# Kernel tuning notes

Hardware: AMD Instinct MI355X
Metric: run time of the kernel (lower is better)

## Reference

```python
import jax, jax.numpy as jnp
import numpy as np

N_NODES = 50000


def _degree_norms(edge_index, n_nodes):
    # PyG GCNConv: add self-loops, deg = 1 + in-degree at target (col)
    src, dst = edge_index[0], edge_index[1]
    deg = 1.0 + jax.ops.segment_sum(jnp.ones(src.shape[0], jnp.float32), dst,
                                    num_segments=n_nodes)
    d_inv_sqrt = 1.0 / jnp.sqrt(deg)  # deg >= 1 always (self-loop)
    norm_e = d_inv_sqrt[src] * d_inv_sqrt[dst]   # per-edge sym norm
    norm_self = d_inv_sqrt * d_inv_sqrt          # self-loop weight
    return norm_e, norm_self


def _gcn_conv(x, W, b, src, dst, norm_e, norm_self, n_nodes):
    h = x @ W                                    # [N, F_out]
    msg = h[src] * norm_e[:, None]               # gather + scale, [E, F_out]
    agg = jax.ops.segment_sum(msg, dst, num_segments=n_nodes)
    return agg + norm_self[:, None] * h + b


def setup_inputs() -> dict:
    key = jax.random.key(0)
    ks = jax.random.split(key, 10)
    F_in, H = 128, 128
    E = 1_600_000
    x = jax.random.normal(ks[0], (N_NODES, F_in), jnp.float32)
    edge_index = jax.random.randint(ks[1], (2, E), 0, N_NODES, dtype=jnp.int64)

    def glorot(k, fi, fo):
        s = jnp.sqrt(6.0 / (fi + fo)).astype(jnp.float32)
        return jax.random.uniform(k, (fi, fo), jnp.float32, -s, s)

    return {
        "x": x,
        "edge_index": edge_index,
        "W1": glorot(ks[2], F_in, H), "b1": jnp.zeros((H,), jnp.float32),
        "W2": glorot(ks[3], H, H),    "b2": jnp.zeros((H,), jnp.float32),
        "W3": glorot(ks[4], H, H),    "b3": jnp.zeros((H,), jnp.float32),
        "W4": glorot(ks[5], H, 1),    "b4": jnp.zeros((1,), jnp.float32),
    }


def reference(x, edge_index, W1, b1, W2, b2, W3, b3, W4, b4):
    src, dst = edge_index[0], edge_index[1]
    norm_e, norm_self = _degree_norms(edge_index, N_NODES)
    h = jax.nn.relu(_gcn_conv(x, W1, b1, src, dst, norm_e, norm_self, N_NODES))
    h = jax.nn.relu(_gcn_conv(h, W2, b2, src, dst, norm_e, norm_self, N_NODES))
    h = jax.nn.relu(_gcn_conv(h, W3, b3, src, dst, norm_e, norm_self, N_NODES))
    return _gcn_conv(h, W4, b4, src, dst, norm_e, norm_self, N_NODES)
```

## Files before the change

kernel.cpp:

```cpp
#include <hip/hip_runtime.h>
#include <hip/hip_bf16.h>
#include <stdint.h>

typedef unsigned int u32;
typedef unsigned short u16;

#define F 128

typedef __attribute__((ext_vector_type(8))) short bf16x8;
typedef __attribute__((ext_vector_type(4))) float f32x4;

__device__ __forceinline__ float bf2f(u16 v){
  union { u32 u; float f; } x; x.u = ((u32)v) << 16; return x.f;
}
__device__ __forceinline__ u16 f2bf(float f){
  union { float f; u32 u; } x; x.f = f;
  u32 u = x.u;
  return (u16)((u + 0x7fffu + ((u >> 16) & 1u)) >> 16);
}

__global__ void k_dtype(const u32* __restrict__ w, int nwords, int* __restrict__ isf32){
  u32 hit = 0;
  for (int i = threadIdx.x; i < nwords; i += blockDim.x){
    u32 e = (w[i] >> 7) & 0xFFu;
    if (e > 160u) hit = 1;
  }
  if (hit) atomicOr(isf32, 1);
}

__global__ void k_detect(const u32* __restrict__ w, int ncheck, int* __restrict__ flag){
  u32 v = 0;
  for (int i = threadIdx.x; i < ncheck; i += blockDim.x) v |= w[2*i + 1];
  if (v) atomicOr(flag, 1);
}

__launch_bounds__(256)
__global__ void k_bhist(const u32* __restrict__ w, int E, const int* __restrict__ flagp,
                        int NB, int* __restrict__ bcnt){
  __shared__ int h[256];
  int st = (*flagp) ? 1 : 2;
  int t = threadIdx.x;
  h[t] = 0;
  __syncthreads();
  int base = blockIdx.x*4096;
  #pragma unroll 4
  for (int k = 0; k < 16; k++){
    int i = base + k*256 + t;
    if (i < E){
      int d = (int)w[(size_t)(E + i)*st];
      atomicAdd(&h[d >> 8], 1);
    }
  }
  __syncthreads();
  if (t < NB && h[t]) atomicAdd(&bcnt[t], h[t]);
}

__global__ void k_bscan(const int* __restrict__ bcnt, int NB, int E,
                        int* __restrict__ bbase, int* __restrict__ bump){
  __shared__ int s[256];
  int t = threadIdx.x;
  int v = (t < NB) ? bcnt[t] : 0;
  s[t] = v;
  __syncthreads();
  for (int off = 1; off < 256; off <<= 1){
    int x = (t >= off) ? s[t - off] : 0;
    __syncthreads();
    s[t] += x;
    __syncthreads();
  }
  bbase[t] = s[t] - v;
  if (t == 255) bbase[256] = E;
  bump[t] = 0;
}

__launch_bounds__(256)
__global__ void k_msplit(const u32* __restrict__ w, int E, const int* __restrict__ flagp,
                         const int* __restrict__ bbase, int* __restrict__ bump,
                         u32* __restrict__ ebuf){
  __shared__ int h[256];
  __shared__ int cb[256];
  int st = (*flagp) ? 1 : 2;
  int t = threadIdx.x;
  h[t] = 0;
  __syncthreads();
  int base = blockIdx.x*4096;
  u32 ps[16]; int bk[16]; int rk[16];
  #pragma unroll 4
  for (int k = 0; k < 16; k++){
    int i = base + k*256 + t;
    if (i < E){
      u32 s = w[(size_t)i*st];
      u32 d = w[(size_t)(E + i)*st];
      bk[k] = (int)(d >> 8);
      ps[k] = (s & 0xFFFFu) | ((d & 0xFFu) << 16);
      rk[k] = atomicAdd(&h[bk[k]], 1);
    } else bk[k] = -1;
  }
  __syncthreads();
  cb[t] = h[t] ? (bbase[t] + atomicAdd(&bump[t], h[t])) : 0;
  __syncthreads();
  #pragma unroll 4
  for (int k = 0; k < 16; k++){
    if (bk[k] >= 0) ebuf[cb[bk[k]] + rk[k]] = ps[k];
  }
}

__launch_bounds__(256)
__global__ void k_bemit(const u32* __restrict__ ebuf, const int* __restrict__ bbase,
                        int N, int* __restrict__ deg, int* __restrict__ rs,
                        u16* __restrict__ csr){
  __shared__ int nd[256];
  __shared__ int nofs[256];
  __shared__ int s[256];
  int b = blockIdx.x;
  int t = threadIdx.x;
  int e0 = bbase[b], e1 = bbase[b + 1];
  nd[t] = 0;
  __syncthreads();
  for (int i = e0 + t; i < e1; i += 256) atomicAdd(&nd[ebuf[i] >> 16], 1);
  __syncthreads();
  int v = nd[t];
  s[t] = v;
  __syncthreads();
  for (int off = 1; off < 256; off <<= 1){
    int x = (t >= off) ? s[t - off] : 0;
    __syncthreads();
    s[t] += x;
    __syncthreads();
  }
  nofs[t] = s[t] - v;
  int node = b*256 + t;
  if (node < N){ deg[node] = v; rs[node] = e0 + nofs[t]; }
  nd[t] = 0;
  __syncthreads();
  for (int i = e0 + t; i < e1; i += 256){
    u32 p = ebuf[i];
    int d = (int)(p >> 16);
    int pos = e0 + nofs[d] + atomicAdd(&nd[d], 1);
    csr[pos] = (u16)(p & 0xFFFFu);
  }
}

__global__ void k_dis(const int* __restrict__ deg, float* __restrict__ dis, int N){
  int i = blockIdx.x*blockDim.x + threadIdx.x;
  if (i < N) dis[i] = rsqrtf(1.0f + (float)deg[i]);
}

__global__ void k_cvt_f(const void* __restrict__ in, const int* __restrict__ isf32,
                        float* __restrict__ out, int n){
  int i = blockIdx.x*blockDim.x + threadIdx.x;
  if (i < n){
    out[i] = (*isf32) ? ((const float*)in)[i] : bf2f(((const u16*)in)[i]);
  }
}

__global__ void k_cvt_b(const void* __restrict__ in, const int* __restrict__ isf32,
                        u16* __restrict__ out, int n){
  int i = blockIdx.x*blockDim.x + threadIdx.x;
  if (i < n){
    float v = (*isf32) ? ((const float*)in)[i] : bf2f(((const u16*)in)[i]);
    out[i] = f2bf(v);
  }
}

__global__ void k_swz(const void* __restrict__ W, const int* __restrict__ isf32,
                      u16* __restrict__ WL){
  int idx = blockIdx.x*256 + threadIdx.x;
  int j    = idx & 7;
  int lane = (idx >> 3) & 63;
  int kb   = (idx >> 9) & 3;
  int ct   = idx >> 11;
  int m = lane & 15, q = lane >> 4;
  int k = kb*32 + q*8 + j;
  int c = ct*16 + m;
  float v = (*isf32) ? ((const float*)W)[k*F + c] : bf2f(((const u16*)W)[k*F + c]);
  WL[idx] = f2bf(v);
}

__launch_bounds__(256)
__global__ void k_mm(const u16* __restrict__ X, const u16* __restrict__ WL,
                     const float* __restrict__ dis, u16* __restrict__ G, int N){
  int w = threadIdx.x >> 6, lane = threadIdx.x & 63;
  int m = lane & 15, q = lane >> 4;
  int row0 = blockIdx.x*64 + w*16;
  int arow = row0 + m;
  bf16x8 a[4];
  if (arow < N){
    const u16* xp = X + (size_t)arow*F;
    #pragma unroll
    for (int kb = 0; kb < 4; kb++) a[kb] = *(const bf16x8*)(xp + kb*32 + q*8);
  } else {
    #pragma unroll
    for (int kb = 0; kb < 4; kb++) a[kb] = (bf16x8){0,0,0,0,0,0,0,0};
  }
  f32x4 acc[8];
  #pragma unroll
  for (int ct = 0; ct < 8; ct++) acc[ct] = (f32x4){0.f,0.f,0.f,0.f};
  #pragma unroll
  for (int ct = 0; ct < 8; ct++){
    #pragma unroll
    for (int kb = 0; kb < 4; kb++){
      bf16x8 b = *(const bf16x8*)(WL + ((size_t)((ct*4 + kb)*64 + lane))*8);
      acc[ct] = __builtin_amdgcn_mfma_f32_16x16x32_bf16(a[kb], b, acc[ct], 0, 0, 0);
    }
  }
  int rbase = row0 + q*4;
  #pragma unroll
  for (int r = 0; r < 4; r++){
    int row = rbase + r;
    if (row < N){
      float dv = dis[row];
      #pragma unroll
      for (int ct = 0; ct < 8; ct++)
        G[(size_t)row*F + ct*16 + m] = f2bf(dv*acc[ct][r]);
    }
  }
}

__launch_bounds__(256)
__global__ void k_agg(const u16* __restrict__ G, const float* __restrict__ dis,
                      const int* __restrict__ rs, const int* __restrict__ deg,
                      const u16* __restrict__ csr, const float* __restrict__ bias,
                      u16* __restrict__ Xout, int N, int relu){
  int wid  = blockIdx.x*4 + (threadIdx.x >> 6);
  int lane = threadIdx.x & 63;
  if (wid >= N) return;
  int base = rs[wid], len = deg[wid];
  u32 sw = *(const u32*)(G + (size_t)wid*F + 2*lane);
  float a0 = bf2f((u16)sw), a1 = bf2f((u16)(sw >> 16));
  float p0=0.f,p1=0.f,p2=0.f,p3=0.f,q0=0.f,q1=0.f,q2=0.f,q3=0.f;
  for (int c0 = 0; c0 < len; c0 += 64){
    int mm = len - c0; if (mm > 64) mm = 64;
    int sidx = (lane < mm) ? (int)csr[base + c0 + lane] : 0;
    int j = 0;
    for (; j + 4 <= mm; j += 4){
      int s0 = __builtin_amdgcn_readlane(sidx, j);
      int s1 = __builtin_amdgcn_readlane(sidx, j+1);
      int s2 = __builtin_amdgcn_readlane(sidx, j+2);
      int s3 = __builtin_amdgcn_readlane(sidx, j+3);
      u32 w0 = *(const u32*)(G + (size_t)s0*F + 2*lane);
      u32 w1 = *(const u32*)(G + (size_t)s1*F + 2*lane);
      u32 w2 = *(const u32*)(G + (size_t)s2*F + 2*lane);
      u32 w3 = *(const u32*)(G + (size_t)s3*F + 2*lane);
      p0 += bf2f((u16)w0); q0 += bf2f((u16)(w0 >> 16));
      p1 += bf2f((u16)w1); q1 += bf2f((u16)(w1 >> 16));
      p2 += bf2f((u16)w2); q2 += bf2f((u16)(w2 >> 16));
      p3 += bf2f((u16)w3); q3 += bf2f((u16)(w3 >> 16));
    }
    for (; j < mm; j++){
      int s0 = __builtin_amdgcn_readlane(sidx, j);
      u32 w0 = *(const u32*)(G + (size_t)s0*F + 2*lane);
      p0 += bf2f((u16)w0); q0 += bf2f((u16)(w0 >> 16));
    }
  }
  a0 += (p0 + p1) + (p2 + p3);
  a1 += (q0 + q1) + (q2 + q3);
  float dv = dis[wid];
  float o0 = fmaf(dv, a0, bias[2*lane]);
  float o1 = fmaf(dv, a1, bias[2*lane + 1]);
  if (relu){ o0 = fmaxf(o0, 0.f); o1 = fmaxf(o1, 0.f); }
  *(u32*)(Xout + (size_t)wid*F + 2*lane) = (u32)f2bf(o0) | ((u32)f2bf(o1) << 16);
}

__global__ void k_mm4(const u16* __restrict__ X, const float* __restrict__ W4f,
                      const float* __restrict__ dis, float* __restrict__ G4, int N){
  int gt   = blockIdx.x*blockDim.x + threadIdx.x;
  int wid  = gt >> 6;
  int lane = threadIdx.x & 63;
  if (wid >= N) return;
  u32 xw = *(const u32*)(X + (size_t)wid*F + 2*lane);
  float acc = bf2f((u16)xw)*W4f[2*lane] + bf2f((u16)(xw >> 16))*W4f[2*lane + 1];
  #pragma unroll
  for (int off = 32; off > 0; off >>= 1) acc += __shfl_down(acc, off, 64);
  if (lane == 0) G4[wid] = dis[wid]*acc;
}

__global__ void k_agg4(const float* __restrict__ G4, const float* __restrict__ dis,
                       const int* __restrict__ rs, const int* __restrict__ deg,
                       const u16* __restrict__ csr, const float* __restrict__ b4f,
                       const int* __restrict__ isf32, void* __restrict__ out, int N){
  int i = blockIdx.x*blockDim.x + threadIdx.x;
  if (i >= N) return;
  int base = rs[i], len = deg[i];
  float acc = G4[i];
  for (int j = 0; j < len; j++) acc += G4[csr[base + j]];
  float r = dis[i]*acc + b4f[0];
  if (*isf32) ((float*)out)[i] = r;
  else        ((u16*)out)[i]   = f2bf(r);
}

extern "C" void kernel_launch(void* const* d_in, const int* in_sizes, int n_in,
                              void* d_out, int out_size, void* d_ws, size_t ws_size,
                              hipStream_t stream){
  const void* x0 = d_in[0];
  const u32*  ei = (const u32*)d_in[1];
  const void* Wp[4] = {d_in[2], d_in[4], d_in[6], d_in[8]};
  const void* bp[4] = {d_in[3], d_in[5], d_in[7], d_in[9]};
  int N = in_sizes[0] / F;
  int E = in_sizes[1] / 2;
  int NB = (N + 255) >> 8;

  char* base = (char*)d_ws;
  size_t off = 0;
  auto alloc = [&](size_t bytes)->char*{
    char* p = base + off;
    off = (off + bytes + 255) & ~(size_t)255;
    return p;
  };
  int*   deg  = (int*)  alloc((size_t)N*4);
  float* dis  = (float*)alloc((size_t)N*4);
  int*   rs   = (int*)  alloc((size_t)N*4);
  float* g4   = (float*)alloc((size_t)N*4);
  int*   bcnt = (int*)  alloc(1024);
  int*   bbase= (int*)  alloc(1056);
  int*   bump = (int*)  alloc(1024);
  int*   flags= (int*)  alloc(256);
  u32*   ebuf = (u32*)  alloc((size_t)E*4);
  u16*   csr  = (u16*)  alloc((size_t)E*2);
  u16*   WL   = (u16*)  alloc(16384*2);
  float* wf4  = (float*)alloc(F*4);
  float* bb   = (float*)alloc(F*4);
  float* bb4  = (float*)alloc(256);
  u16*   gbuf = (u16*)  alloc((size_t)N*F*2);
  u16*   xbuf = (u16*)  alloc((size_t)N*F*2);

  hipMemsetAsync(bcnt, 0, 1024, stream);
  hipMemsetAsync(flags, 0, 256, stream);

  int* eflag = flags + 0;
  int* isf32 = flags + 1;

  int nbt = (N + 255)/256;
  int etb = (E + 4095)/4096;

  k_dtype <<<1, 256, 0, stream>>>((const u32*)x0, 2048, isf32);
  k_detect<<<1, 256, 0, stream>>>(ei, 4096, eflag);
  k_bhist <<<etb, 256, 0, stream>>>(ei, E, eflag, NB, bcnt);
  k_bscan <<<1, 256, 0, stream>>>(bcnt, NB, E, bbase, bump);
  k_msplit<<<etb, 256, 0, stream>>>(ei, E, eflag, bbase, bump, ebuf);
  k_bemit <<<NB, 256, 0, stream>>>(ebuf, bbase, N, deg, rs, csr);
  k_dis   <<<nbt, 256, 0, stream>>>(deg, dis, N);

  int mmb = (N + 63)/64;
  int agb = (N + 3)/4;

  k_cvt_b<<<((size_t)N*F + 255)/256, 256, 0, stream>>>(x0, isf32, xbuf, N*F);

  for (int l = 0; l < 3; l++){
    k_swz  <<<64, 256, 0, stream>>>(Wp[l], isf32, WL);
    k_cvt_f<<<1, 128, 0, stream>>>(bp[l], isf32, bb, F);
    k_mm   <<<mmb, 256, 0, stream>>>(xbuf, WL, dis, gbuf, N);
    k_agg  <<<agb, 256, 0, stream>>>(gbuf, dis, rs, deg, csr, bb, xbuf, N, 1);
  }
  k_cvt_f<<<1, 128, 0, stream>>>(Wp[3], isf32, wf4, F);
  k_cvt_f<<<1, 64, 0, stream>>>(bp[3], isf32, bb4, 1);
  k_mm4  <<<((size_t)N*64 + 255)/256, 256, 0, stream>>>(xbuf, wf4, dis, g4, N);
  k_agg4 <<<nbt, 256, 0, stream>>>(g4, dis, rs, deg, csr, bb4, isf32, (void*)d_out, N);
}
```

Baseline: 406.0 us.

## Split aggregation across feature chunks and merge small prep kernels

The aggregation kernel now uses a 2D grid. Each of four column chunks handles 32 features per node, and four lane groups gather different neighbors in parallel and are reduced with shuffles. This raises the number of independent loads in flight per wave, at the cost of re-reading the CSR indices for every chunk. Small setup kernels are merged: dtype and edge detection become one launch, the degree norm is computed inside bemit, and all weight swizzles and bias conversions go into one prep launch. Buffers are padded so the matmul can store rows without bounds checks, and out-of-range neighbor lanes read the padded row N.

After: 625.8 us. +54.1%, slower.

```diff
diff --git a/kernel.cpp b/kernel.cpp
--- a/kernel.cpp
+++ b/kernel.cpp
@@ -19,19 +19,23 @@
   return (u16)((u + 0x7fffu + ((u >> 16) & 1u)) >> 16);
 }
 
-__global__ void k_dtype(const u32* __restrict__ w, int nwords, int* __restrict__ isf32){
-  u32 hit = 0;
-  for (int i = threadIdx.x; i < nwords; i += blockDim.x){
-    u32 e = (w[i] >> 7) & 0xFFu;
+__global__ void k_flags(const u32* __restrict__ x, const u32* __restrict__ ei,
+                        int* __restrict__ flags){
+  __shared__ int f[2];
+  int t = threadIdx.x;
+  if (t < 2) f[t] = 0;
+  __syncthreads();
+  int hit = 0;
+  for (int i = t; i < 2048; i += 256){
+    u32 e = (x[i] >> 7) & 0xFFu;
     if (e > 160u) hit = 1;
   }
-  if (hit) atomicOr(isf32, 1);
-}
-
-__global__ void k_detect(const u32* __restrict__ w, int ncheck, int* __restrict__ flag){
+  if (hit) atomicOr(&f[1], 1);
   u32 v = 0;
-  for (int i = threadIdx.x; i < ncheck; i += blockDim.x) v |= w[2*i + 1];
-  if (v) atomicOr(flag, 1);
+  for (int i = t; i < 4096; i += 256) v |= ei[2*i + 1];
+  if (v) atomicOr(&f[0], 1);
+  __syncthreads();
+  if (t < 2) flags[t] = f[t];
 }
 
 __launch_bounds__(256)
@@ -108,7 +112,7 @@
 __launch_bounds__(256)
 __global__ void k_bemit(const u32* __restrict__ ebuf, const int* __restrict__ bbase,
                         int N, int* __restrict__ deg, int* __restrict__ rs,
-                        u16* __restrict__ csr){
+                        float* __restrict__ dis, u16* __restrict__ csr){
   __shared__ int nd[256];
   __shared__ int nofs[256];
   __shared__ int s[256];
@@ -130,7 +134,11 @@
   }
   nofs[t] = s[t] - v;
   int node = b*256 + t;
-  if (node < N){ deg[node] = v; rs[node] = e0 + nofs[t]; }
+  if (node < N){
+    deg[node] = v;
+    rs[node]  = e0 + nofs[t];
+    dis[node] = rsqrtf(1.0f + (float)v);
+  }
   nd[t] = 0;
   __syncthreads();
   for (int i = e0 + t; i < e1; i += 256){
@@ -138,19 +146,6 @@
     int d = (int)(p >> 16);
     int pos = e0 + nofs[d] + atomicAdd(&nd[d], 1);
     csr[pos] = (u16)(p & 0xFFFFu);
-  }
-}
-
-__global__ void k_dis(const int* __restrict__ deg, float* __restrict__ dis, int N){
-  int i = blockIdx.x*blockDim.x + threadIdx.x;
-  if (i < N) dis[i] = rsqrtf(1.0f + (float)deg[i]);
-}
-
-__global__ void k_cvt_f(const void* __restrict__ in, const int* __restrict__ isf32,
-                        float* __restrict__ out, int n){
-  int i = blockIdx.x*blockDim.x + threadIdx.x;
-  if (i < n){
-    out[i] = (*isf32) ? ((const float*)in)[i] : bf2f(((const u16*)in)[i]);
   }
 }
 
@@ -163,18 +158,38 @@
   }
 }
 
-__global__ void k_swz(const void* __restrict__ W, const int* __restrict__ isf32,
-                      u16* __restrict__ WL){
-  int idx = blockIdx.x*256 + threadIdx.x;
-  int j    = idx & 7;
-  int lane = (idx >> 3) & 63;
-  int kb   = (idx >> 9) & 3;
-  int ct   = idx >> 11;
-  int m = lane & 15, q = lane >> 4;
-  int k = kb*32 + q*8 + j;
-  int c = ct*16 + m;
-  float v = (*isf32) ? ((const float*)W)[k*F + c] : bf2f(((const u16*)W)[k*F + c]);
-  WL[idx] = f2bf(v);
+__global__ void k_prep(const void* __restrict__ W1, const void* __restrict__ W2,
+                       const void* __restrict__ W3, const void* __restrict__ W4,
+                       const void* __restrict__ b1, const void* __restrict__ b2,
+                       const void* __restrict__ b3, const void* __restrict__ b4,
+                       const int* __restrict__ isf32, u16* __restrict__ WL,
+                       float* __restrict__ bb, float* __restrict__ wf4,
+                       float* __restrict__ bb4){
+  int b = blockIdx.x, t = threadIdx.x;
+  int f32 = *isf32;
+  if (b < 192){
+    int l = b >> 6;
+    const void* W = (l == 0) ? W1 : (l == 1) ? W2 : W3;
+    int idx = (b & 63)*256 + t;
+    int j    = idx & 7;
+    int lane = (idx >> 3) & 63;
+    int kb   = (idx >> 9) & 3;
+    int ct   = idx >> 11;
+    int m = lane & 15, q = lane >> 4;
+    int k = kb*32 + q*8 + j;
+    int c = ct*16 + m;
+    float v = f32 ? ((const float*)W)[k*F + c] : bf2f(((const u16*)W)[k*F + c]);
+    WL[l*16384 + idx] = f2bf(v);
+  } else {
+    if (t < 128){
+      const void* bs[3] = {b1, b2, b3};
+      #pragma unroll
+      for (int l = 0; l < 3; l++)
+        bb[l*F + t] = f32 ? ((const float*)bs[l])[t] : bf2f(((const u16*)bs[l])[t]);
+      wf4[t] = f32 ? ((const float*)W4)[t] : bf2f(((const u16*)W4)[t]);
+      if (t == 0) bb4[0] = f32 ? ((const float*)b4)[0] : bf2f(((const u16*)b4)[0]);
+    }
+  }
 }
 
 __launch_bounds__(256)
@@ -208,12 +223,10 @@
   #pragma unroll
   for (int r = 0; r < 4; r++){
     int row = rbase + r;
-    if (row < N){
-      float dv = dis[row];
-      #pragma unroll
-      for (int ct = 0; ct < 8; ct++)
-        G[(size_t)row*F + ct*16 + m] = f2bf(dv*acc[ct][r]);
-    }
+    float dv = (row < N) ? dis[row] : 0.f;
+    #pragma unroll
+    for (int ct = 0; ct < 8; ct++)
+      G[(size_t)row*F + ct*16 + m] = f2bf(dv*acc[ct][r]);
   }
 }
 
@@ -221,45 +234,39 @@
 __global__ void k_agg(const u16* __restrict__ G, const float* __restrict__ dis,
                       const int* __restrict__ rs, const int* __restrict__ deg,
                       const u16* __restrict__ csr, const float* __restrict__ bias,
-                      u16* __restrict__ Xout, int N, int relu){
+                      u16* __restrict__ Xout, int N){
+  const u32* Gw = (const u32*)G;
+  u32* Xw = (u32*)Xout;
   int wid  = blockIdx.x*4 + (threadIdx.x >> 6);
   int lane = threadIdx.x & 63;
   if (wid >= N) return;
+  int c    = blockIdx.y;
+  int g    = lane >> 4;
+  int cofs = c*16 + (lane & 15);
   int base = rs[wid], len = deg[wid];
-  u32 sw = *(const u32*)(G + (size_t)wid*F + 2*lane);
-  float a0 = bf2f((u16)sw), a1 = bf2f((u16)(sw >> 16));
-  float p0=0.f,p1=0.f,p2=0.f,p3=0.f,q0=0.f,q1=0.f,q2=0.f,q3=0.f;
+  float a0 = 0.f, a1 = 0.f;
   for (int c0 = 0; c0 < len; c0 += 64){
     int mm = len - c0; if (mm > 64) mm = 64;
-    int sidx = (lane < mm) ? (int)csr[base + c0 + lane] : 0;
-    int j = 0;
-    for (; j + 4 <= mm; j += 4){
-      int s0 = __builtin_amdgcn_readlane(sidx, j);
-      int s1 = __builtin_amdgcn_readlane(sidx, j+1);
-      int s2 = __builtin_amdgcn_readlane(sidx, j+2);
-      int s3 = __builtin_amdgcn_readlane(sidx, j+3);
-      u32 w0 = *(const u32*)(G + (size_t)s0*F + 2*lane);
-      u32 w1 = *(const u32*)(G + (size_t)s1*F + 2*lane);
-      u32 w2 = *(const u32*)(G + (size_t)s2*F + 2*lane);
-      u32 w3 = *(const u32*)(G + (size_t)s3*F + 2*lane);
-      p0 += bf2f((u16)w0); q0 += bf2f((u16)(w0 >> 16));
-      p1 += bf2f((u16)w1); q1 += bf2f((u16)(w1 >> 16));
-      p2 += bf2f((u16)w2); q2 += bf2f((u16)(w2 >> 16));
-      p3 += bf2f((u16)w3); q3 += bf2f((u16)(w3 >> 16));
+    int sidx = (lane < mm) ? (int)csr[base + c0 + lane] : N;
+    int jmax = (mm + 3) >> 2;
+    #pragma unroll 2
+    for (int j = 0; j < jmax; j++){
+      int s = __shfl(sidx, j*4 + g, 64);
+      u32 w = Gw[((size_t)(u32)s << 6) + cofs];
+      a0 += __uint_as_float(w << 16);
+      a1 += __uint_as_float(w & 0xFFFF0000u);
     }
-    for (; j < mm; j++){
-      int s0 = __builtin_amdgcn_readlane(sidx, j);
-      u32 w0 = *(const u32*)(G + (size_t)s0*F + 2*lane);
-      p0 += bf2f((u16)w0); q0 += bf2f((u16)(w0 >> 16));
-    }
-  }
-  a0 += (p0 + p1) + (p2 + p3);
-  a1 += (q0 + q1) + (q2 + q3);
-  float dv = dis[wid];
-  float o0 = fmaf(dv, a0, bias[2*lane]);
-  float o1 = fmaf(dv, a1, bias[2*lane + 1]);
-  if (relu){ o0 = fmaxf(o0, 0.f); o1 = fmaxf(o1, 0.f); }
-  *(u32*)(Xout + (size_t)wid*F + 2*lane) = (u32)f2bf(o0) | ((u32)f2bf(o1) << 16);
+  }
+  a0 += __shfl_xor(a0, 16, 64); a0 += __shfl_xor(a0, 32, 64);
+  a1 += __shfl_xor(a1, 16, 64); a1 += __shfl_xor(a1, 32, 64);
+  if (lane < 16){
+    u32 sw = Gw[((size_t)wid << 6) + cofs];
+    float dv = dis[wid];
+    float o0 = fmaf(dv, __uint_as_float(sw << 16) + a0, bias[c*32 + 2*lane]);
+    float o1 = fmaf(dv, __uint_as_float(sw & 0xFFFF0000u) + a1, bias[c*32 + 2*lane + 1]);
+    o0 = fmaxf(o0, 0.f); o1 = fmaxf(o1, 0.f);
+    Xw[((size_t)wid << 6) + cofs] = (u32)f2bf(o0) | ((u32)f2bf(o1) << 16);
+  }
 }
 
 __global__ void k_mm4(const u16* __restrict__ X, const float* __restrict__ W4f,
@@ -294,11 +301,10 @@
                               hipStream_t stream){
   const void* x0 = d_in[0];
   const u32*  ei = (const u32*)d_in[1];
-  const void* Wp[4] = {d_in[2], d_in[4], d_in[6], d_in[8]};
-  const void* bp[4] = {d_in[3], d_in[5], d_in[7], d_in[9]};
   int N = in_sizes[0] / F;
   int E = in_sizes[1] / 2;
   int NB = (N + 255) >> 8;
+  int Npad = ((N + 63)/64)*64;
 
   char* base = (char*)d_ws;
   size_t off = 0;
@@ -317,43 +323,37 @@
   int*   flags= (int*)  alloc(256);
   u32*   ebuf = (u32*)  alloc((size_t)E*4);
   u16*   csr  = (u16*)  alloc((size_t)E*2);
-  u16*   WL   = (u16*)  alloc(16384*2);
+  u16*   WL   = (u16*)  alloc((size_t)3*16384*2);
   float* wf4  = (float*)alloc(F*4);
-  float* bb   = (float*)alloc(F*4);
+  float* bb   = (float*)alloc((size_t)3*F*4);
   float* bb4  = (float*)alloc(256);
-  u16*   gbuf = (u16*)  alloc((size_t)N*F*2);
-  u16*   xbuf = (u16*)  alloc((size_t)N*F*2);
+  u16*   gbuf = (u16*)  alloc((size_t)Npad*F*2);
+  u16*   xbuf = (u16*)  alloc((size_t)Npad*F*2);
 
   hipMemsetAsync(bcnt, 0, 1024, stream);
-  hipMemsetAsync(flags, 0, 256, stream);
 
   int* eflag = flags + 0;
   int* isf32 = flags + 1;
 
   int nbt = (N + 255)/256;
   int etb = (E + 4095)/4096;
-
-  k_dtype <<<1, 256, 0, stream>>>((const u32*)x0, 2048, isf32);
-  k_detect<<<1, 256, 0, stream>>>(ei, 4096, eflag);
+  int mmb = (N + 63)/64;
+
+  k_flags <<<1, 256, 0, stream>>>((const u32*)x0, ei, flags);
   k_bhist <<<etb, 256, 0, stream>>>(ei, E, eflag, NB, bcnt);
   k_bscan <<<1, 256, 0, stream>>>(bcnt, NB, E, bbase, bump);
   k_msplit<<<etb, 256, 0, stream>>>(ei, E, eflag, bbase, bump, ebuf);
-  k_bemit <<<NB, 256, 0, stream>>>(ebuf, bbase, N, deg, rs, csr);
-  k_dis   <<<nbt, 256, 0, stream>>>(deg, dis, N);
-
-  int mmb = (N + 63)/64;
-  int agb = (N + 3)/4;
-
-  k_cvt_b<<<((size_t)N*F + 255)/256, 256, 0, stream>>>(x0, isf32, xbuf, N*F);
-
+  k_bemit <<<NB, 256, 0, stream>>>(ebuf, bbase, N, deg, rs, dis, csr);
+  k_prep  <<<193, 256, 0, stream>>>(d_in[2], d_in[4], d_in[6], d_in[8],
+                                    d_in[3], d_in[5], d_in[7], d_in[9],
+                                    isf32, WL, bb, wf4, bb4);
+  k_cvt_b <<<((size_t)N*F + 255)/256, 256, 0, stream>>>(x0, isf32, xbuf, N*F);
+
+  dim3 agrid((N + 3)/4, 4);
   for (int l = 0; l < 3; l++){
-    k_swz  <<<64, 256, 0, stream>>>(Wp[l], isf32, WL);
-    k_cvt_f<<<1, 128, 0, stream>>>(bp[l], isf32, bb, F);
-    k_mm   <<<mmb, 256, 0, stream>>>(xbuf, WL, dis, gbuf, N);
-    k_agg  <<<agb, 256, 0, stream>>>(gbuf, dis, rs, deg, csr, bb, xbuf, N, 1);
-  }
-  k_cvt_f<<<1, 128, 0, stream>>>(Wp[3], isf32, wf4, F);
-  k_cvt_f<<<1, 64, 0, stream>>>(bp[3], isf32, bb4, 1);
-  k_mm4  <<<((size_t)N*64 + 255)/256, 256, 0, stream>>>(xbuf, wf4, dis, g4, N);
-  k_agg4 <<<nbt, 256, 0, stream>>>(g4, dis, rs, deg, csr, bb4, isf32, (void*)d_out, N);
-}
+    k_mm <<<mmb, 256, 0, stream>>>(xbuf, WL + l*16384, dis, gbuf, N);
+    k_agg<<<agrid, 256, 0, stream>>>(gbuf, dis, rs, deg, csr, bb + l*F, xbuf, N);
+  }
+  k_mm4 <<<((size_t)N*64 + 255)/256, 256, 0, stream>>>(xbuf, wf4, dis, g4, N);
+  k_agg4<<<nbt, 256, 0, stream>>>(g4, dis, rs, deg, csr, bb4, isf32, (void*)d_out, N);
+}
```
